# Optimization experiments

Measured on AMD Instinct MI355X. Metric: run time of the kernel, lower is better.

The kernel has to match this reference:

```python
import jax, jax.numpy as jnp
import numpy as np

S, B, E, D, H, F, L = 1024, 8, 768, 8, 8, 2048, 4
D = 1024  # HIDDEN_DIM
H = 8     # nhead
DH = D // H
EPS = 1e-5


def _ln(x, g, b):
    m = jnp.mean(x, -1, keepdims=True)
    v = jnp.mean(jnp.square(x - m), -1, keepdims=True)
    return (x - m) * jax.lax.rsqrt(v + EPS) * g + b


def setup_inputs() -> dict:
    key = jax.random.key(0)
    ks = iter(jax.random.split(key, 16))
    n = lambda shape: jax.random.normal(next(ks), shape, jnp.float32) * 0.02
    return dict(
        x=jax.random.normal(next(ks), (S, B, E), jnp.float32),
        enc_w=n((D, E)), enc_b=jnp.zeros((D,), jnp.float32),
        enc_ln_g=jnp.ones((D,), jnp.float32), enc_ln_b=jnp.zeros((D,), jnp.float32),
        qkv_w=n((L, 3 * D, D)), qkv_b=jnp.zeros((L, 3 * D), jnp.float32),
        out_w=n((L, D, D)), out_b=jnp.zeros((L, D), jnp.float32),
        ln1_g=jnp.ones((L, D), jnp.float32), ln1_b=jnp.zeros((L, D), jnp.float32),
        ff1_w=n((L, F, D)), ff1_b=jnp.zeros((L, F), jnp.float32),
        ff2_w=n((L, D, F)), ff2_b=jnp.zeros((L, D), jnp.float32),
        ln2_g=jnp.ones((L, D), jnp.float32), ln2_b=jnp.zeros((L, D), jnp.float32),
        dec_w1=n((D // 2, D)), dec_b1=jnp.zeros((D // 2,), jnp.float32),
        dec_ln_g=jnp.ones((D // 2,), jnp.float32), dec_ln_b=jnp.zeros((D // 2,), jnp.float32),
        dec_w2=n((E, D // 2)), dec_b2=jnp.zeros((E,), jnp.float32),
    )


def reference(x, enc_w, enc_b, enc_ln_g, enc_ln_b, qkv_w, qkv_b, out_w, out_b,
              ln1_g, ln1_b, ff1_w, ff1_b, ff2_w, ff2_b, ln2_g, ln2_b,
              dec_w1, dec_b1, dec_ln_g, dec_ln_b, dec_w2, dec_b2):
    # encoder MLP: Linear -> LayerNorm -> ReLU (dropout = identity at eval)
    h = jax.nn.relu(_ln(x @ enc_w.T + enc_b, enc_ln_g, enc_ln_b))  # (S,B,D)
    scale = np.float32(1.0 / np.sqrt(DH))
    for l in range(L):  # 4 post-norm TransformerEncoderLayers, eager attention
        qkv = h @ qkv_w[l].T + qkv_b[l]                    # (S,B,3D)
        q, k, v = jnp.split(qkv, 3, axis=-1)
        q = q.reshape(S, B, H, DH)
        k = k.reshape(S, B, H, DH)
        v = v.reshape(S, B, H, DH)
        scores = jnp.einsum('sbhd,tbhd->bhst', q, k) * scale  # (B,H,S,S)
        p = jax.nn.softmax(scores, axis=-1)
        o = jnp.einsum('bhst,tbhd->sbhd', p, v).reshape(S, B, D)
        o = o @ out_w[l].T + out_b[l]
        h = _ln(h + o, ln1_g[l], ln1_b[l])
        f = jax.nn.relu(h @ ff1_w[l].T + ff1_b[l]) @ ff2_w[l].T + ff2_b[l]
        h = _ln(h + f, ln2_g[l], ln2_b[l])
    # decoder MLP
    d = jax.nn.relu(_ln(h @ dec_w1.T + dec_b1, dec_ln_g, dec_ln_b))
    return d @ dec_w2.T + dec_b2  # (S,B,E)
```

## Files before the change

### kernel.cpp

```cpp
#include <hip/hip_runtime.h>
#include <math.h>

#define S_ 1024
#define B_ 8
#define E_ 768
#define D_ 1024
#define H_ 8
#define F_ 2048
#define L_ 4
#define M_ (S_*B_)

typedef unsigned short u16;
typedef unsigned int u32;
typedef u16 u16x8 __attribute__((ext_vector_type(8)));
typedef u16 u16x4 __attribute__((ext_vector_type(4)));
typedef u16 u16x2 __attribute__((ext_vector_type(2)));
typedef u32 u32x2 __attribute__((ext_vector_type(2)));
typedef short bf16x8 __attribute__((ext_vector_type(8)));
typedef float f32x4 __attribute__((ext_vector_type(4)));

#define AS1 __attribute__((address_space(1)))
#define AS3 __attribute__((address_space(3)))

#define QSCALE 0.127517432f

__device__ __forceinline__ void gload_lds16(const void* g, void* l) {
  __builtin_amdgcn_global_load_lds((const AS1 void*)g, (AS3 void*)l, 16, 0, 0);
}
__device__ __forceinline__ u16 f2bf(float f) {
  unsigned u = __builtin_bit_cast(unsigned, f);
  return (u16)((u + 0x7fffu + ((u >> 16) & 1u)) >> 16);
}
__device__ __forceinline__ float bf2f(u16 h) {
  unsigned u = ((unsigned)h) << 16;
  return __builtin_bit_cast(float, u);
}
__device__ __forceinline__ u32 cvtpk(float a, float b) {
  u32 r;
  asm("v_cvt_pk_bf16_f32 %0, %1, %2" : "=v"(r) : "v"(a), "v"(b));
  return r;
}

__global__ __launch_bounds__(256) void conv4(
    const float* __restrict__ s0, u16* __restrict__ d0, int n0,
    const float* __restrict__ s1, u16* __restrict__ d1, int n1,
    const float* __restrict__ s2, u16* __restrict__ d2, int n2,
    const float* __restrict__ s3, u16* __restrict__ d3, int n3)
{
  int total = (n0 + n1 + n2 + n3) >> 2;
  for (int i = blockIdx.x * 256 + threadIdx.x; i < total; i += gridDim.x * 256) {
    int e = i << 2;
    const float* s; u16* d; int off;
    if (e < n0)           { s = s0; d = d0; off = e; }
    else if (e < n0+n1)   { s = s1; d = d1; off = e - n0; }
    else if (e < n0+n1+n2){ s = s2; d = d2; off = e - n0 - n1; }
    else                  { s = s3; d = d3; off = e - n0 - n1 - n2; }
    float4 v = *(const float4*)&s[off];
    u16x4 o; o[0]=f2bf(v.x); o[1]=f2bf(v.y); o[2]=f2bf(v.z); o[3]=f2bf(v.w);
    *(u16x4*)&d[off] = o;
  }
}

template<int ACT, int OUTBF, int SCQ, int RES>
__global__ __launch_bounds__(512) void gemm256(
    const u16* __restrict__ A, const u16* __restrict__ W,
    const float* __restrict__ bias, const u16* __restrict__ Rres,
    void* __restrict__ Cout, int M, int N, int K)
{
  __shared__ u16 lds[73728];
  const int gx = gridDim.x, nwg = gx * gridDim.y;
  const int lin = blockIdx.y * gx + blockIdx.x;
  const int work = (lin & 7) * (nwg >> 3) + (lin >> 3);
  const int bm = (work / gx) * 256, bn = (work % gx) * 128;
  const int tid = threadIdx.x;
  const int l = tid & 63;
  const int w = tid >> 6;
  const int l15 = l & 15, lg = l >> 4;
  const int wr = w & 3, wc = w >> 2;
  const int srow = tid >> 3;
  const int scb  = tid & 7;

  f32x4 acc[4][4] = {};
  const int nt = K >> 6;

#define STAGE(c, k0)                                                        \
  {                                                                         \
    u16* Ab = lds + (c)*24576;                                              \
    u16* Bb = Ab + 16384;                                                   \
    _Pragma("unroll")                                                       \
    for (int u = 0; u < 4; ++u) {                                           \
      int row = u*64 + srow;                                                \
      int cb  = scb ^ (row & 7);                                            \
      gload_lds16(A + (size_t)(bm + row) * K + (k0) + cb*8,                 \
                  Ab + u*4096 + tid*8);                                     \
    }                                                                       \
    _Pragma("unroll")                                                       \
    for (int u = 0; u < 2; ++u) {                                           \
      int row = u*64 + srow;                                                \
      int cb  = scb ^ (row & 7);                                            \
      gload_lds16(W + (size_t)(bn + row) * K + (k0) + cb*8,                 \
                  Bb + u*4096 + tid*8);                                     \
    }                                                                       \
  }

  STAGE(0, 0);
  STAGE(1, 64);
  asm volatile("s_waitcnt vmcnt(6)" ::: "memory");
  __builtin_amdgcn_s_barrier();

  int cr = 0, cw = 2;
  for (int t = 0; t < nt; ++t) {
    if (t + 2 < nt) STAGE(cw, (t + 2) << 6);
    const u16* Ab = lds + cr*24576;
    const u16* Bb = Ab + 16384;
    #pragma unroll
    for (int ks = 0; ks < 2; ++ks) {
      bf16x8 af[4], bf_[4];
      #pragma unroll
      for (int mi = 0; mi < 4; ++mi) {
        int row = wr*64 + mi*16 + l15;
        af[mi] = *(const bf16x8*)&Ab[row*64 + ((ks*4 + lg) ^ (row & 7))*8];
      }
      #pragma unroll
      for (int ni = 0; ni < 4; ++ni) {
        int row = wc*64 + ni*16 + l15;
        bf_[ni] = *(const bf16x8*)&Bb[row*64 + ((ks*4 + lg) ^ (row & 7))*8];
      }
      #pragma unroll
      for (int mi = 0; mi < 4; ++mi)
        #pragma unroll
        for (int ni = 0; ni < 4; ++ni)
          acc[mi][ni] = __builtin_amdgcn_mfma_f32_16x16x32_bf16(af[mi], bf_[ni], acc[mi][ni], 0, 0, 0);
    }
    if (t + 1 < nt) {
      if (t + 2 < nt) { asm volatile("s_waitcnt vmcnt(6)" ::: "memory"); }
      else            { asm volatile("s_waitcnt vmcnt(0)" ::: "memory"); }
      __builtin_amdgcn_s_barrier();
    }
    cr = (cr == 2) ? 0 : cr + 1;
    cw = (cw == 2) ? 0 : cw + 1;
  }
#undef STAGE

  u16* Cb = (u16*)Cout; float* Cf = (float*)Cout;
  #pragma unroll
  for (int ni = 0; ni < 4; ++ni) {
    int col = bn + wc*64 + ni*16 + l15;
    float bv = bias[col];
    #pragma unroll
    for (int mi = 0; mi < 4; ++mi) {
      #pragma unroll
      for (int rr = 0; rr < 4; ++rr) {
        int row = bm + wr*64 + mi*16 + lg*4 + rr;
        float v = acc[mi][ni][rr] + bv;
        if (RES) v += bf2f(Rres[(size_t)row * N + col]);
        if (ACT) v = fmaxf(v, 0.f);
        if (SCQ) { if (col < 1024) v *= QSCALE; }
        if (OUTBF) Cb[(size_t)row * N + col] = f2bf(v);
        else       Cf[(size_t)row * N + col] = v;
      }
    }
  }
}

template<int ACT, int OUTBF, int SCQ>
__global__ __launch_bounds__(256) void gemm_mfma(
    const u16* __restrict__ A, const u16* __restrict__ W,
    const float* __restrict__ bias, void* __restrict__ Cout,
    int M, int N, int K)
{
  __shared__ u16 As[128*32];
  __shared__ u16 Bs[128*32];
  const int gx = gridDim.x, nwg = gx * gridDim.y;
  const int lin = blockIdx.y * gx + blockIdx.x;
  const int work = (lin & 7) * (nwg >> 3) + (lin >> 3);
  const int bm = (work / gx) * 128, bn = (work % gx) * 128;
  const int tid = threadIdx.x;
  const int w = tid >> 6, l = tid & 63;
  const int l15 = l & 15, lg = l >> 4;
  const int wr = w >> 1, wc = w & 1;
  f32x4 acc[4][4] = {};

  for (int k0 = 0; k0 < K; k0 += 32) {
    __syncthreads();
    #pragma unroll
    for (int j = 0; j < 2; ++j) {
      int e = (w*2 + j) * 512 + l * 8;
      int row = e >> 5, ko = (l & 3) * 8;
      gload_lds16(A + (size_t)(bm + row) * K + k0 + ko, &As[(w*2 + j) * 512]);
      gload_lds16(W + (size_t)(bn + row) * K + k0 + ko, &Bs[(w*2 + j) * 512]);
    }
    __syncthreads();
    bf16x8 af[4], bf_[4];
    #pragma unroll
    for (int mi = 0; mi < 4; ++mi) {
      int row = wr*64 + mi*16 + l15;
      af[mi] = *(const bf16x8*)&As[row*32 + lg*8];
    }
    #pragma unroll
    for (int ni = 0; ni < 4; ++ni) {
      int row = wc*64 + ni*16 + l15;
      bf_[ni] = *(const bf16x8*)&Bs[row*32 + lg*8];
    }
    #pragma unroll
    for (int mi = 0; mi < 4; ++mi)
      #pragma unroll
      for (int ni = 0; ni < 4; ++ni)
        acc[mi][ni] = __builtin_amdgcn_mfma_f32_16x16x32_bf16(af[mi], bf_[ni], acc[mi][ni], 0, 0, 0);
  }

  u16* Cb = (u16*)Cout; float* Cf = (float*)Cout;
  #pragma unroll
  for (int ni = 0; ni < 4; ++ni) {
    int col = bn + wc*64 + ni*16 + l15;
    float bv = bias[col];
    #pragma unroll
    for (int mi = 0; mi < 4; ++mi) {
      #pragma unroll
      for (int rr = 0; rr < 4; ++rr) {
        int row = bm + wr*64 + mi*16 + lg*4 + rr;
        float v = acc[mi][ni][rr] + bv;
        if (ACT) v = fmaxf(v, 0.f);
        if (SCQ) { if (col < 1024) v *= QSCALE; }
        if (OUTBF) Cb[(size_t)row * N + col] = f2bf(v);
        else       Cf[(size_t)row * N + col] = v;
      }
    }
  }
}

template<int NV, bool RESID, bool RELU>
__global__ __launch_bounds__(256) void ln_bf16(
    const u16* __restrict__ X, const u16* __restrict__ R,
    const float* __restrict__ g, const float* __restrict__ b,
    u16* __restrict__ Y)
{
  constexpr int D = NV * 256;
  __shared__ float sbuf[8];
  const int tid = threadIdx.x;
  const size_t base = (size_t)blockIdx.x * D + tid * NV;
  float v[NV];
  if constexpr (NV == 4) {
    u16x4 xv = *(const u16x4*)&X[base];
    #pragma unroll
    for (int i = 0; i < 4; ++i) v[i] = bf2f(xv[i]);
    if (RESID) {
      u16x4 rv = *(const u16x4*)&R[base];
      #pragma unroll
      for (int i = 0; i < 4; ++i) v[i] += bf2f(rv[i]);
    }
  } else {
    u16x2 xv = *(const u16x2*)&X[base];
    #pragma unroll
    for (int i = 0; i < 2; ++i) v[i] = bf2f(xv[i]);
    if (RESID) {
      u16x2 rv = *(const u16x2*)&R[base];
      #pragma unroll
      for (int i = 0; i < 2; ++i) v[i] += bf2f(rv[i]);
    }
  }
  float sum = 0.f, sq = 0.f;
  #pragma unroll
  for (int i = 0; i < NV; ++i) { sum += v[i]; sq += v[i]*v[i]; }
  #pragma unroll
  for (int off = 32; off > 0; off >>= 1) {
    sum += __shfl_down(sum, off);
    sq  += __shfl_down(sq, off);
  }
  if ((tid & 63) == 0) { sbuf[tid >> 6] = sum; sbuf[4 + (tid >> 6)] = sq; }
  __syncthreads();
  sum = sbuf[0] + sbuf[1] + sbuf[2] + sbuf[3];
  sq  = sbuf[4] + sbuf[5] + sbuf[6] + sbuf[7];
  const float mean = sum / (float)D;
  const float rstd = rsqrtf(sq / (float)D - mean*mean + 1e-5f);
  const int c0 = tid * NV;
  if constexpr (NV == 4) {
    u16x4 o;
    #pragma unroll
    for (int i = 0; i < 4; ++i) {
      float t = (v[i] - mean) * rstd * g[c0+i] + b[c0+i];
      if (RELU) t = fmaxf(t, 0.f);
      o[i] = f2bf(t);
    }
    *(u16x4*)&Y[base] = o;
  } else {
    u16x2 o;
    #pragma unroll
    for (int i = 0; i < 2; ++i) {
      float t = (v[i] - mean) * rstd * g[c0+i] + b[c0+i];
      if (RELU) t = fmaxf(t, 0.f);
      o[i] = f2bf(t);
    }
    *(u16x2*)&Y[base] = o;
  }
}

__global__ __launch_bounds__(256) void vtrans(
    const u16* __restrict__ QKV, u16* __restrict__ Vt)
{
  __shared__ u16 Ls[32*132];
  const int st = blockIdx.x, bh = blockIdx.y;
  const int bb = bh >> 3, hh = bh & 7;
  const int t = threadIdx.x;
  #pragma unroll
  for (int i = 0; i < 2; ++i) {
    int e = i*256 + t;
    int s = e >> 4, d0 = (e & 15) * 8;
    u16x8 v = *(const u16x8*)&QKV[(size_t)((st*32 + s)*8 + bb)*3072 + 2048 + hh*128 + d0];
    #pragma unroll
    for (int j = 0; j < 4; ++j) {
      u16x2 p; p[0] = v[2*j]; p[1] = v[2*j+1];
      *(u16x2*)&Ls[s*132 + d0 + 2*j] = p;
    }
  }
  __syncthreads();
  #pragma unroll
  for (int i = 0; i < 2; ++i) {
    int e = i*256 + t;
    int d = e >> 2, s0 = (e & 3) * 8;
    u16x8 v;
    #pragma unroll
    for (int j = 0; j < 8; ++j) v[j] = Ls[(s0+j)*132 + d];
    *(u16x8*)&Vt[(size_t)bh*131072 + (size_t)d*1024 + st*32 + s0] = v;
  }
}

__global__ __launch_bounds__(512, 4) void attn_mfma(
    const u16* __restrict__ QKV, const u16* __restrict__ Vt,
    u16* __restrict__ AO)
{
  __shared__ u16 Ks[2][64*128];
  __shared__ u16 Vs[2][128*64];
  __shared__ u16 Pl[8][16*64];
  const int bid = blockIdx.x;
  const int wg = (bid & 7) * 64 + (bid >> 3);
  const int qt = wg & 7, bh = wg >> 3;
  const int bb = bh >> 3, hh = bh & 7;
  const int tid = threadIdx.x, w = tid >> 6, l = tid & 63;
  const int l15 = l & 15, lg = l >> 4;

  bf16x8 aq[4];
  {
    int q = qt*128 + w*16 + l15;
    const u16* qp = QKV + (size_t)(q*8 + bb)*3072 + hh*128 + lg*8;
    #pragma unroll
    for (int kc = 0; kc < 4; ++kc)
      aq[kc] = *(const bf16x8*)(qp + kc*32);
  }
  const u16* vbase = Vt + (size_t)bh*131072;

#define STAGE_KV(c, kt)                                                     \
  {                                                                         \
    _Pragma("unroll")                                                       \
    for (int i = 0; i < 2; ++i) {                                           \
      int e = (w*2 + i) * 512 + l * 8;                                      \
      int krow = e >> 7, d0 = e & 127;                                      \
      int dsw = d0 ^ ((krow & 7) << 3);                                     \
      gload_lds16(QKV + (size_t)(((kt)*64 + krow)*8 + bb)*3072 + 1024       \
                      + hh*128 + dsw,                                       \
                  &Ks[c][(w*2 + i) * 512]);                                 \
      int vd = e >> 6, vc = e & 63;                                         \
      int vsw = vc ^ ((vd & 7) << 3);                                       \
      gload_lds16(vbase + (size_t)vd*1024 + (kt)*64 + vsw,                  \
                  &Vs[c][(w*2 + i) * 512]);                                 \
    }                                                                       \
  }

  f32x4 of[8] = {};
  float mreg = -INFINITY, lpart = 0.f;
  const int psw = (l15 & 7) << 3;

  STAGE_KV(0, 0);
  __syncthreads();

  for (int kt = 0; kt < 16; ++kt) {
    const int cur = kt & 1;
    if (kt + 1 < 16) STAGE_KV(cur ^ 1, kt + 1);

    f32x4 sf[4] = {};
    __builtin_amdgcn_s_setprio(1);
    #pragma unroll
    for (int kc = 0; kc < 4; ++kc) {
      #pragma unroll
      for (int f = 0; f < 4; ++f) {
        int krow = f*16 + l15;
        bf16x8 bk = *(const bf16x8*)&Ks[cur][krow*128 + ((kc*32 + lg*8) ^ ((krow & 7) << 3))];
        sf[f] = __builtin_amdgcn_mfma_f32_16x16x32_bf16(bk, aq[kc], sf[f], 0, 0, 0);
      }
    }
    __builtin_amdgcn_s_setprio(0);

    float pm01 = fmaxf(fmaxf(sf[0][0], sf[0][1]), fmaxf(sf[0][2], sf[0][3]));
    float pm23 = fmaxf(fmaxf(sf[1][0], sf[1][1]), fmaxf(sf[1][2], sf[1][3]));
    float pm45 = fmaxf(fmaxf(sf[2][0], sf[2][1]), fmaxf(sf[2][2], sf[2][3]));
    float pm67 = fmaxf(fmaxf(sf[3][0], sf[3][1]), fmaxf(sf[3][2], sf[3][3]));
    float pmax = fmaxf(fmaxf(pm01, pm23), fmaxf(pm45, pm67));
    pmax = fmaxf(pmax, __shfl_xor(pmax, 16));
    pmax = fmaxf(pmax, __shfl_xor(pmax, 32));

    if (__any(pmax > mreg + 8.f)) {
      float mn = fmaxf(mreg, pmax);
      float al = exp2f(mreg - mn);
      mreg = mn;
      lpart *= al;
      #pragma unroll
      for (int r = 0; r < 4; ++r) {
        float alq = __shfl(al, (l & 48) + lg*4 + r);
        #pragma unroll
        for (int ni = 0; ni < 8; ++ni) of[ni][r] *= alq;
      }
    }

    float psum = 0.f;
    #pragma unroll
    for (int f = 0; f < 4; ++f) {
      float p0 = exp2f(sf[f][0] - mreg);
      float p1 = exp2f(sf[f][1] - mreg);
      float p2 = exp2f(sf[f][2] - mreg);
      float p3 = exp2f(sf[f][3] - mreg);
      psum += (p0 + p1) + (p2 + p3);
      u32x2 pk; pk[0] = cvtpk(p0, p1); pk[1] = cvtpk(p2, p3);
      *(u32x2*)&Pl[w][l15*64 + ((f*16 + lg*4) ^ psw)] = pk;
    }
    lpart += psum;

    bf16x8 pa0 = *(const bf16x8*)&Pl[w][l15*64 + ((lg*8) ^ psw)];
    bf16x8 pa1 = *(const bf16x8*)&Pl[w][l15*64 + ((32 + lg*8) ^ psw)];
    __builtin_amdgcn_s_setprio(1);
    #pragma unroll
    for (int ni = 0; ni < 8; ++ni) {
      int n = ni*16 + l15;
      int nsw = (n & 7) << 3;
      bf16x8 vb0 = *(const bf16x8*)&Vs[cur][n*64 + ((lg*8) ^ nsw)];
      bf16x8 vb1 = *(const bf16x8*)&Vs[cur][n*64 + ((32 + lg*8) ^ nsw)];
      of[ni] = __builtin_amdgcn_mfma_f32_16x16x32_bf16(pa0, vb0, of[ni], 0, 0, 0);
      of[ni] = __builtin_amdgcn_mfma_f32_16x16x32_bf16(pa1, vb1, of[ni], 0, 0, 0);
    }
    __builtin_amdgcn_s_setprio(0);

    if (kt + 1 < 16) __syncthreads();
  }
#undef STAGE_KV

  float ls = lpart;
  ls += __shfl_xor(ls, 16);
  ls += __shfl_xor(ls, 32);
  float inv = 1.f / ls;
  #pragma unroll
  for (int r = 0; r < 4; ++r) {
    float invq = __shfl(inv, (l & 48) + lg*4 + r);
    int q = qt*128 + w*16 + lg*4 + r;
    size_t base = (size_t)(q*8 + bb) * 1024 + hh*128;
    #pragma unroll
    for (int ni = 0; ni < 8; ++ni)
      AO[base + ni*16 + l15] = f2bf(of[ni][r] * invq);
  }
}

#define O_WENC  0ull
#define O_WDEC1 786432ull
#define O_WDEC2 1310720ull
#define O_WLQ   1703936ull
#define O_WLO   4849664ull
#define O_WLF1  5898240ull
#define O_WLF2  7995392ull
#define O_R     10092544ull
#define O_H     35258368ull
#define O_AO    43646976ull
#define O_VT    52035584ull

extern "C" void kernel_launch(void* const* d_in, const int* in_sizes, int n_in,
                              void* d_out, int out_size, void* d_ws, size_t ws_size,
                              hipStream_t stream) {
  (void)in_sizes; (void)n_in; (void)out_size; (void)ws_size;
  const float* x        = (const float*)d_in[0];
  const float* enc_w    = (const float*)d_in[1];
  const float* enc_b    = (const float*)d_in[2];
  const float* enc_ln_g = (const float*)d_in[3];
  const float* enc_ln_b = (const float*)d_in[4];
  const float* qkv_w    = (const float*)d_in[5];
  const float* qkv_b    = (const float*)d_in[6];
  const float* out_w    = (const float*)d_in[7];
  const float* out_b    = (const float*)d_in[8];
  const float* ln1_g    = (const float*)d_in[9];
  const float* ln1_b    = (const float*)d_in[10];
  const float* ff1_w    = (const float*)d_in[11];
  const float* ff1_b    = (const float*)d_in[12];
  const float* ff2_w    = (const float*)d_in[13];
  const float* ff2_b    = (const float*)d_in[14];
  const float* ln2_g    = (const float*)d_in[15];
  const float* ln2_b    = (const float*)d_in[16];
  const float* dec_w1   = (const float*)d_in[17];
  const float* dec_b1   = (const float*)d_in[18];
  const float* dec_ln_g = (const float*)d_in[19];
  const float* dec_ln_b = (const float*)d_in[20];
  const float* dec_w2   = (const float*)d_in[21];
  const float* dec_b2   = (const float*)d_in[22];

  u16* ws16 = (u16*)d_ws;
  u16* wenc  = ws16 + O_WENC;
  u16* wdec1 = ws16 + O_WDEC1;
  u16* wdec2 = ws16 + O_WDEC2;
  u16* wlq   = ws16 + O_WLQ;
  u16* wlo   = ws16 + O_WLO;
  u16* wlf1  = ws16 + O_WLF1;
  u16* wlf2  = ws16 + O_WLF2;
  u16* qkv   = ws16 + O_R;
  u16* bufY  = ws16 + O_R;
  u16* bufG  = ws16 + O_R + 8388608ull;
  u16* xb    = bufG;
  u16* dech  = bufG;
  u16* h     = ws16 + O_H;
  u16* ao    = ws16 + O_AO;
  u16* vt    = ws16 + O_VT;

  const dim3 blk(256);
  const dim3 blk5(512);

  conv4<<<1024, blk, 0, stream>>>(x, xb, 8192*768,
                                  enc_w, wenc, 1024*768,
                                  dec_w1, wdec1, 512*1024,
                                  dec_w2, wdec2, 768*512);
  gemm_mfma<0,1,0><<<dim3(8,64), blk, 0, stream>>>(xb, wenc, enc_b, bufY, M_, 1024, 768);
  ln_bf16<4,false,true><<<M_, blk, 0, stream>>>(bufY, nullptr, enc_ln_g, enc_ln_b, h);

  for (int l = 0; l < L_; ++l) {
    conv4<<<1024, blk, 0, stream>>>(qkv_w + (size_t)l*3145728, wlq, 3145728,
                                    out_w + (size_t)l*1048576, wlo, 1048576,
                                    ff1_w + (size_t)l*2097152, wlf1, 2097152,
                                    ff2_w + (size_t)l*2097152, wlf2, 2097152);
    gemm256<0,1,1,0><<<dim3(24,32), blk5, 0, stream>>>(h, wlq, qkv_b + (size_t)l*3072, nullptr, qkv, M_, 3072, 1024);
    vtrans<<<dim3(32,64), blk, 0, stream>>>(qkv, vt);
    attn_mfma<<<512, blk5, 0, stream>>>(qkv, vt, ao);
    gemm256<0,1,0,1><<<dim3(8,32), blk5, 0, stream>>>(ao, wlo, out_b + (size_t)l*1024, h, bufY, M_, 1024, 1024);
    ln_bf16<4,false,false><<<M_, blk, 0, stream>>>(bufY, nullptr, ln1_g + (size_t)l*1024, ln1_b + (size_t)l*1024, h);
    gemm256<1,1,0,0><<<dim3(16,32), blk5, 0, stream>>>(h, wlf1, ff1_b + (size_t)l*2048, nullptr, bufG, M_, 2048, 1024);
    gemm256<0,1,0,1><<<dim3(8,32), blk5, 0, stream>>>(bufG, wlf2, ff2_b + (size_t)l*1024, h, bufY, M_, 1024, 2048);
    ln_bf16<4,false,false><<<M_, blk, 0, stream>>>(bufY, nullptr, ln2_g + (size_t)l*1024, ln2_b + (size_t)l*1024, h);
  }

  gemm_mfma<0,1,0><<<dim3(4,64), blk, 0, stream>>>(h, wdec1, dec_b1, bufY, M_, 512, 1024);
  ln_bf16<2,false,true><<<M_, blk, 0, stream>>>(bufY, nullptr, dec_ln_g, dec_ln_b, dech);
  gemm_mfma<0,0,0><<<dim3(6,64), blk, 0, stream>>>(dech, wdec2, dec_b2, d_out, M_, 768, 512);
}
```

Measured before the change: 1.084 ms.

## Replace 256x128 GEMM with 128x128 triple-buffered swizzled GEMM, drop attention setprio

Removes the 512-thread 256x128 GEMM and the simple 128x128 GEMM and replaces both with one 256-thread 128x128 kernel. It uses a 32-wide K tile, three LDS stages loaded by direct global-to-LDS copies, and an XOR swizzle on reads. The smaller tile uses less LDS, which allows more workgroups per CU and a larger grid, but each tile gets less reuse and needs more barriers. The s_setprio hints around the MFMA loops in the attention kernel are also removed.

```diff
diff --git a/kernel.cpp b/kernel.cpp
--- a/kernel.cpp
+++ b/kernel.cpp
@@ -62,152 +62,77 @@
 }
 
 template<int ACT, int OUTBF, int SCQ, int RES>
-__global__ __launch_bounds__(512) void gemm256(
+__global__ __launch_bounds__(256) void gemm128(
     const u16* __restrict__ A, const u16* __restrict__ W,
     const float* __restrict__ bias, const u16* __restrict__ Rres,
     void* __restrict__ Cout, int M, int N, int K)
 {
-  __shared__ u16 lds[73728];
-  const int gx = gridDim.x, nwg = gx * gridDim.y;
-  const int lin = blockIdx.y * gx + blockIdx.x;
-  const int work = (lin & 7) * (nwg >> 3) + (lin >> 3);
-  const int bm = (work / gx) * 256, bn = (work % gx) * 128;
-  const int tid = threadIdx.x;
-  const int l = tid & 63;
-  const int w = tid >> 6;
-  const int l15 = l & 15, lg = l >> 4;
-  const int wr = w & 3, wc = w >> 2;
-  const int srow = tid >> 3;
-  const int scb  = tid & 7;
-
-  f32x4 acc[4][4] = {};
-  const int nt = K >> 6;
-
-#define STAGE(c, k0)                                                        \
-  {                                                                         \
-    u16* Ab = lds + (c)*24576;                                              \
-    u16* Bb = Ab + 16384;                                                   \
-    _Pragma("unroll")                                                       \
-    for (int u = 0; u < 4; ++u) {                                           \
-      int row = u*64 + srow;                                                \
-      int cb  = scb ^ (row & 7);                                            \
-      gload_lds16(A + (size_t)(bm + row) * K + (k0) + cb*8,                 \
-                  Ab + u*4096 + tid*8);                                     \
-    }                                                                       \
-    _Pragma("unroll")                                                       \
-    for (int u = 0; u < 2; ++u) {                                           \
-      int row = u*64 + srow;                                                \
-      int cb  = scb ^ (row & 7);                                            \
-      gload_lds16(W + (size_t)(bn + row) * K + (k0) + cb*8,                 \
-                  Bb + u*4096 + tid*8);                                     \
-    }                                                                       \
-  }
-
-  STAGE(0, 0);
-  STAGE(1, 64);
-  asm volatile("s_waitcnt vmcnt(6)" ::: "memory");
-  __builtin_amdgcn_s_barrier();
-
-  int cr = 0, cw = 2;
-  for (int t = 0; t < nt; ++t) {
-    if (t + 2 < nt) STAGE(cw, (t + 2) << 6);
-    const u16* Ab = lds + cr*24576;
-    const u16* Bb = Ab + 16384;
-    #pragma unroll
-    for (int ks = 0; ks < 2; ++ks) {
-      bf16x8 af[4], bf_[4];
-      #pragma unroll
-      for (int mi = 0; mi < 4; ++mi) {
-        int row = wr*64 + mi*16 + l15;
-        af[mi] = *(const bf16x8*)&Ab[row*64 + ((ks*4 + lg) ^ (row & 7))*8];
-      }
-      #pragma unroll
-      for (int ni = 0; ni < 4; ++ni) {
-        int row = wc*64 + ni*16 + l15;
-        bf_[ni] = *(const bf16x8*)&Bb[row*64 + ((ks*4 + lg) ^ (row & 7))*8];
-      }
-      #pragma unroll
-      for (int mi = 0; mi < 4; ++mi)
-        #pragma unroll
-        for (int ni = 0; ni < 4; ++ni)
-          acc[mi][ni] = __builtin_amdgcn_mfma_f32_16x16x32_bf16(af[mi], bf_[ni], acc[mi][ni], 0, 0, 0);
-    }
-    if (t + 1 < nt) {
-      if (t + 2 < nt) { asm volatile("s_waitcnt vmcnt(6)" ::: "memory"); }
-      else            { asm volatile("s_waitcnt vmcnt(0)" ::: "memory"); }
-      __builtin_amdgcn_s_barrier();
-    }
-    cr = (cr == 2) ? 0 : cr + 1;
-    cw = (cw == 2) ? 0 : cw + 1;
-  }
-#undef STAGE
-
-  u16* Cb = (u16*)Cout; float* Cf = (float*)Cout;
-  #pragma unroll
-  for (int ni = 0; ni < 4; ++ni) {
-    int col = bn + wc*64 + ni*16 + l15;
-    float bv = bias[col];
-    #pragma unroll
-    for (int mi = 0; mi < 4; ++mi) {
-      #pragma unroll
-      for (int rr = 0; rr < 4; ++rr) {
-        int row = bm + wr*64 + mi*16 + lg*4 + rr;
-        float v = acc[mi][ni][rr] + bv;
-        if (RES) v += bf2f(Rres[(size_t)row * N + col]);
-        if (ACT) v = fmaxf(v, 0.f);
-        if (SCQ) { if (col < 1024) v *= QSCALE; }
-        if (OUTBF) Cb[(size_t)row * N + col] = f2bf(v);
-        else       Cf[(size_t)row * N + col] = v;
-      }
-    }
-  }
-}
-
-template<int ACT, int OUTBF, int SCQ>
-__global__ __launch_bounds__(256) void gemm_mfma(
-    const u16* __restrict__ A, const u16* __restrict__ W,
-    const float* __restrict__ bias, void* __restrict__ Cout,
-    int M, int N, int K)
-{
-  __shared__ u16 As[128*32];
-  __shared__ u16 Bs[128*32];
+  __shared__ u16 lds[24576];
   const int gx = gridDim.x, nwg = gx * gridDim.y;
   const int lin = blockIdx.y * gx + blockIdx.x;
   const int work = (lin & 7) * (nwg >> 3) + (lin >> 3);
   const int bm = (work / gx) * 128, bn = (work % gx) * 128;
   const int tid = threadIdx.x;
-  const int w = tid >> 6, l = tid & 63;
+  const int l = tid & 63;
+  const int w = tid >> 6;
   const int l15 = l & 15, lg = l >> 4;
   const int wr = w >> 1, wc = w & 1;
+  const int srow = tid >> 2;
+  const int scb  = tid & 3;
+
   f32x4 acc[4][4] = {};
-
-  for (int k0 = 0; k0 < K; k0 += 32) {
-    __syncthreads();
-    #pragma unroll
-    for (int j = 0; j < 2; ++j) {
-      int e = (w*2 + j) * 512 + l * 8;
-      int row = e >> 5, ko = (l & 3) * 8;
-      gload_lds16(A + (size_t)(bm + row) * K + k0 + ko, &As[(w*2 + j) * 512]);
-      gload_lds16(W + (size_t)(bn + row) * K + k0 + ko, &Bs[(w*2 + j) * 512]);
-    }
-    __syncthreads();
+  const int nt = K >> 5;
+
+#define STAGE(c, k0)                                                        \
+  {                                                                         \
+    u16* Ab = lds + (c)*8192;                                               \
+    u16* Bb = Ab + 4096;                                                    \
+    _Pragma("unroll")                                                       \
+    for (int u = 0; u < 2; ++u) {                                           \
+      int row = u*64 + srow;                                                \
+      int cb  = scb ^ (row & 3);                                            \
+      gload_lds16(A + (size_t)(bm + row) * K + (k0) + cb*8,                 \
+                  Ab + u*2048 + tid*8);                                     \
+      gload_lds16(W + (size_t)(bn + row) * K + (k0) + cb*8,                 \
+                  Bb + u*2048 + tid*8);                                     \
+    }                                                                       \
+  }
+
+  STAGE(0, 0);
+  STAGE(1, 32);
+  asm volatile("s_waitcnt vmcnt(4)" ::: "memory");
+  __builtin_amdgcn_s_barrier();
+
+  int cr = 0, cw = 2;
+  for (int t = 0; t < nt; ++t) {
+    if (t + 2 < nt) STAGE(cw, (t + 2) << 5);
+    const u16* Ab = lds + cr*8192;
+    const u16* Bb = Ab + 4096;
     bf16x8 af[4], bf_[4];
     #pragma unroll
     for (int mi = 0; mi < 4; ++mi) {
       int row = wr*64 + mi*16 + l15;
-      af[mi] = *(const bf16x8*)&As[row*32 + lg*8];
+      af[mi] = *(const bf16x8*)&Ab[row*32 + (lg ^ (row & 3))*8];
     }
     #pragma unroll
     for (int ni = 0; ni < 4; ++ni) {
       int row = wc*64 + ni*16 + l15;
-      bf_[ni] = *(const bf16x8*)&Bs[row*32 + lg*8];
+      bf_[ni] = *(const bf16x8*)&Bb[row*32 + (lg ^ (row & 3))*8];
     }
     #pragma unroll
     for (int mi = 0; mi < 4; ++mi)
       #pragma unroll
       for (int ni = 0; ni < 4; ++ni)
         acc[mi][ni] = __builtin_amdgcn_mfma_f32_16x16x32_bf16(af[mi], bf_[ni], acc[mi][ni], 0, 0, 0);
-  }
+    if (t + 1 < nt) {
+      if (t + 2 < nt) { asm volatile("s_waitcnt vmcnt(4)" ::: "memory"); }
+      else            { asm volatile("s_waitcnt vmcnt(0)" ::: "memory"); }
+      __builtin_amdgcn_s_barrier();
+    }
+    cr = (cr == 2) ? 0 : cr + 1;
+    cw = (cw == 2) ? 0 : cw + 1;
+  }
+#undef STAGE
 
   u16* Cb = (u16*)Cout; float* Cf = (float*)Cout;
   #pragma unroll
@@ -220,6 +145,7 @@
       for (int rr = 0; rr < 4; ++rr) {
         int row = bm + wr*64 + mi*16 + lg*4 + rr;
         float v = acc[mi][ni][rr] + bv;
+        if (RES) v += bf2f(Rres[(size_t)row * N + col]);
         if (ACT) v = fmaxf(v, 0.f);
         if (SCQ) { if (col < 1024) v *= QSCALE; }
         if (OUTBF) Cb[(size_t)row * N + col] = f2bf(v);
@@ -378,7 +304,6 @@
     if (kt + 1 < 16) STAGE_KV(cur ^ 1, kt + 1);
 
     f32x4 sf[4] = {};
-    __builtin_amdgcn_s_setprio(1);
     #pragma unroll
     for (int kc = 0; kc < 4; ++kc) {
       #pragma unroll
@@ -388,7 +313,6 @@
         sf[f] = __builtin_amdgcn_mfma_f32_16x16x32_bf16(bk, aq[kc], sf[f], 0, 0, 0);
       }
     }
-    __builtin_amdgcn_s_setprio(0);
 
     float pm01 = fmaxf(fmaxf(sf[0][0], sf[0][1]), fmaxf(sf[0][2], sf[0][3]));
     float pm23 = fmaxf(fmaxf(sf[1][0], sf[1][1]), fmaxf(sf[1][2], sf[1][3]));
@@ -426,7 +350,6 @@
 
     bf16x8 pa0 = *(const bf16x8*)&Pl[w][l15*64 + ((lg*8) ^ psw)];
     bf16x8 pa1 = *(const bf16x8*)&Pl[w][l15*64 + ((32 + lg*8) ^ psw)];
-    __builtin_amdgcn_s_setprio(1);
     #pragma unroll
     for (int ni = 0; ni < 8; ++ni) {
       int n = ni*16 + l15;
@@ -436,7 +359,6 @@
       of[ni] = __builtin_amdgcn_mfma_f32_16x16x32_bf16(pa0, vb0, of[ni], 0, 0, 0);
       of[ni] = __builtin_amdgcn_mfma_f32_16x16x32_bf16(pa1, vb1, of[ni], 0, 0, 0);
     }
-    __builtin_amdgcn_s_setprio(0);
 
     if (kt + 1 < 16) __syncthreads();
   }
@@ -521,7 +443,7 @@
                                   enc_w, wenc, 1024*768,
                                   dec_w1, wdec1, 512*1024,
                                   dec_w2, wdec2, 768*512);
-  gemm_mfma<0,1,0><<<dim3(8,64), blk, 0, stream>>>(xb, wenc, enc_b, bufY, M_, 1024, 768);
+  gemm128<0,1,0,0><<<dim3(8,64), blk, 0, stream>>>(xb, wenc, enc_b, nullptr, bufY, M_, 1024, 768);
   ln_bf16<4,false,true><<<M_, blk, 0, stream>>>(bufY, nullptr, enc_ln_g, enc_ln_b, h);
 
   for (int l = 0; l < L_; ++l) {
@@ -529,17 +451,17 @@
                                     out_w + (size_t)l*1048576, wlo, 1048576,
                                     ff1_w + (size_t)l*2097152, wlf1, 2097152,
                                     ff2_w + (size_t)l*2097152, wlf2, 2097152);
-    gemm256<0,1,1,0><<<dim3(24,32), blk5, 0, stream>>>(h, wlq, qkv_b + (size_t)l*3072, nullptr, qkv, M_, 3072, 1024);
+    gemm128<0,1,1,0><<<dim3(24,64), blk, 0, stream>>>(h, wlq, qkv_b + (size_t)l*3072, nullptr, qkv, M_, 3072, 1024);
     vtrans<<<dim3(32,64), blk, 0, stream>>>(qkv, vt);
     attn_mfma<<<512, blk5, 0, stream>>>(qkv, vt, ao);
-    gemm256<0,1,0,1><<<dim3(8,32), blk5, 0, stream>>>(ao, wlo, out_b + (size_t)l*1024, h, bufY, M_, 1024, 1024);
+    gemm128<0,1,0,1><<<dim3(8,64), blk, 0, stream>>>(ao, wlo, out_b + (size_t)l*1024, h, bufY, M_, 1024, 1024);
     ln_bf16<4,false,false><<<M_, blk, 0, stream>>>(bufY, nullptr, ln1_g + (size_t)l*1024, ln1_b + (size_t)l*1024, h);
-    gemm256<1,1,0,0><<<dim3(16,32), blk5, 0, stream>>>(h, wlf1, ff1_b + (size_t)l*2048, nullptr, bufG, M_, 2048, 1024);
-    gemm256<0,1,0,1><<<dim3(8,32), blk5, 0, stream>>>(bufG, wlf2, ff2_b + (size_t)l*1024, h, bufY, M_, 1024, 2048);
+    gemm128<1,1,0,0><<<dim3(16,64), blk, 0, stream>>>(h, wlf1, ff1_b + (size_t)l*2048, nullptr, bufG, M_, 2048, 1024);
+    gemm128<0,1,0,1><<<dim3(8,64), blk, 0, stream>>>(bufG, wlf2, ff2_b + (size_t)l*1024, h, bufY, M_, 1024, 2048);
     ln_bf16<4,false,false><<<M_, blk, 0, stream>>>(bufY, nullptr, ln2_g + (size_t)l*1024, ln2_b + (size_t)l*1024, h);
   }
 
-  gemm_mfma<0,1,0><<<dim3(4,64), blk, 0, stream>>>(h, wdec1, dec_b1, bufY, M_, 512, 1024);
+  gemm128<0,1,0,0><<<dim3(4,64), blk, 0, stream>>>(h, wdec1, dec_b1, nullptr, bufY, M_, 512, 1024);
   ln_bf16<2,false,true><<<M_, blk, 0, stream>>>(bufY, nullptr, dec_ln_g, dec_ln_b, dech);
-  gemm_mfma<0,0,0><<<dim3(6,64), blk, 0, stream>>>(dech, wdec2, dec_b2, d_out, M_, 768, 512);
-}
+  gemm128<0,0,0,0><<<dim3(6,64), blk, 0, stream>>>(dech, wdec2, dec_b2, nullptr, d_out, M_, 768, 512);
+}
```

New measurement: 1.139 ms. +5.1%, slower.
